# Performance work log

Measured on AMD Instinct MI355X. Metric: run time of the kernel, lower is better.

## Reference

```python
import jax, jax.numpy as jnp
import numpy as np

ALPHA = 0.2  # LeakyReLU negative slope
N, F_IN, F_OUT = 8192, 512, 64
NEG_INF = -9e15


def setup_inputs() -> dict:
    key = jax.random.key(0)
    k1, k2, k3, k4 = jax.random.split(key, 4)
    inp = jax.random.normal(k1, (N, F_IN), dtype=jnp.float32)
    adj = jax.random.randint(k2, (N, N), 0, 2, dtype=jnp.int32)
    W = jax.random.normal(k3, (F_IN, F_OUT), dtype=jnp.float32) * (1.414 / np.sqrt(F_IN))
    a = jax.random.normal(k4, (2 * F_OUT, 1), dtype=jnp.float32) * 0.1
    return {"input": inp, "adj": adj, "W": W, "a": a, "sparse": 0}


def reference(input, adj, W, a, sparse):
    h = input @ W  # [N, F_out]
    # Decompose concat([h_i, h_j]) @ a into additive src/dst terms (same math,
    # avoids the O(N^2 * 2F) intermediate): e_ij = leakyrelu(h_i@a1 + h_j@a2)
    f_src = h @ a[:F_OUT]   # [N, 1]
    f_dst = h @ a[F_OUT:]   # [N, 1]
    e = jax.nn.leaky_relu(f_src + f_dst.T, ALPHA)  # [N, N]
    attention = jnp.where(adj > 0, e, NEG_INF)
    attention = jax.nn.softmax(attention, axis=1)
    h_prime = attention @ h  # [N, F_out]
    return jax.nn.leaky_relu(h_prime, 0.01)[None]  # concat=True path; default F.leaky_relu slope 0.01
```

## Files before the change

kernel.cpp:

```cpp
#include <hip/hip_runtime.h>
#include <hip/hip_bf16.h>

#define N 8192
#define FIN 512
#define FOUT 64
#define ALPHA 0.2f

typedef __bf16 bf16x8 __attribute__((ext_vector_type(8)));
typedef float f32x4 __attribute__((ext_vector_type(4)));
typedef int i32x4 __attribute__((ext_vector_type(4)));

constexpr int JC = 512;
constexpr int NCH = N / JC;
constexpr int STR = JC + 8;


__device__ __forceinline__ unsigned enc_f(float x) {
    unsigned u = __float_as_uint(x);
    return (u & 0x80000000u) ? ~u : (u | 0x80000000u);
}
__device__ __forceinline__ float dec_f(unsigned u) {
    return (u & 0x80000000u) ? __uint_as_float(u & 0x7FFFFFFFu) : __uint_as_float(~u);
}

__global__ __launch_bounds__(64) void k_wt(const float* __restrict__ W,
                                           __bf16* __restrict__ WtG) {
    const int g = blockIdx.x * 64 + threadIdx.x;
    const int k = g >> 3;
    const int f0 = (g & 7) * 8;
    const float4 w0 = *(const float4*)(W + (size_t)k * FOUT + f0);
    const float4 w1 = *(const float4*)(W + (size_t)k * FOUT + f0 + 4);
    WtG[(size_t)(f0 + 0) * FIN + k] = (__bf16)w0.x;
    WtG[(size_t)(f0 + 1) * FIN + k] = (__bf16)w0.y;
    WtG[(size_t)(f0 + 2) * FIN + k] = (__bf16)w0.z;
    WtG[(size_t)(f0 + 3) * FIN + k] = (__bf16)w0.w;
    WtG[(size_t)(f0 + 4) * FIN + k] = (__bf16)w1.x;
    WtG[(size_t)(f0 + 5) * FIN + k] = (__bf16)w1.y;
    WtG[(size_t)(f0 + 6) * FIN + k] = (__bf16)w1.z;
    WtG[(size_t)(f0 + 7) * FIN + k] = (__bf16)w1.w;
}

__global__ __launch_bounds__(64) void k12(const float* __restrict__ in,
                                          const __bf16* __restrict__ WtG,
                                          const float* __restrict__ a,
                                          float* __restrict__ f_src,
                                          float* __restrict__ f_dst,
                                          unsigned* __restrict__ Mkey,
                                          __bf16* __restrict__ hT) {
    __shared__ __bf16 tb[64][16];
    const int lane = threadIdx.x;
    const int m = lane & 15, quad = lane >> 4;
    const int i0 = blockIdx.x * 16;

    f32x4 acc[4];
#pragma unroll
    for (int t = 0; t < 4; ++t) acc[t] = (f32x4){0.f, 0.f, 0.f, 0.f};

    const float* arow = in + (size_t)(i0 + m) * FIN + quad * 8;
    for (int k0 = 0; k0 < FIN; k0 += 32) {
        const float4 x0 = *(const float4*)(arow + k0);
        const float4 x1 = *(const float4*)(arow + k0 + 4);
        bf16x8 af;
        af[0] = (__bf16)x0.x; af[1] = (__bf16)x0.y; af[2] = (__bf16)x0.z; af[3] = (__bf16)x0.w;
        af[4] = (__bf16)x1.x; af[5] = (__bf16)x1.y; af[6] = (__bf16)x1.z; af[7] = (__bf16)x1.w;
#pragma unroll
        for (int t = 0; t < 4; ++t) {
            const bf16x8 bf = *(const bf16x8*)(WtG + (size_t)(t * 16 + m) * FIN + k0 + quad * 8);
            acc[t] = __builtin_amdgcn_mfma_f32_16x16x32_bf16(af, bf, acc[t], 0, 0, 0);
        }
    }
    float s1[4], s2[4];
#pragma unroll
    for (int r = 0; r < 4; ++r) { s1[r] = 0.f; s2[r] = 0.f; }
#pragma unroll
    for (int t = 0; t < 4; ++t) {
        const float a1 = a[t * 16 + m], a2 = a[64 + t * 16 + m];
#pragma unroll
        for (int r = 0; r < 4; ++r) {
            s1[r] += acc[t][r] * a1;
            s2[r] += acc[t][r] * a2;
        }
    }
#pragma unroll
    for (int off = 1; off <= 8; off <<= 1)
#pragma unroll
        for (int r = 0; r < 4; ++r) {
            s1[r] += __shfl_xor(s1[r], off);
            s2[r] += __shfl_xor(s2[r], off);
        }
    float lm = -1e30f;
    if (m == 0) {
#pragma unroll
        for (int r = 0; r < 4; ++r) {
            f_src[i0 + quad * 4 + r] = s1[r];
            f_dst[i0 + quad * 4 + r] = s2[r];
            lm = fmaxf(lm, s2[r]);
        }
    }
    lm = fmaxf(lm, __shfl_xor(lm, 16));
    lm = fmaxf(lm, __shfl_xor(lm, 32));
    if (lane == 0) atomicMax(Mkey, enc_f(lm));

#pragma unroll
    for (int t = 0; t < 4; ++t)
#pragma unroll
        for (int r = 0; r < 4; ++r) tb[t * 16 + m][quad * 4 + r] = (__bf16)acc[t][r];
    __syncthreads();
    {
        const int f = lane;
        const bf16x8 v0 = *(const bf16x8*)&tb[f][0];
        const bf16x8 v1 = *(const bf16x8*)&tb[f][8];
        *(bf16x8*)(hT + (size_t)f * N + i0) = v0;
        *(bf16x8*)(hT + (size_t)f * N + i0 + 8) = v1;
    }
}

__global__ __launch_bounds__(256) void k3_attn(const int* __restrict__ adj,
                                               const float* __restrict__ f_src,
                                               const float* __restrict__ fdstG,
                                               const unsigned* __restrict__ Mkey,
                                               const __bf16* __restrict__ hT,
                                               float* __restrict__ pnum,
                                               float* __restrict__ plsum) {
    __shared__ __bf16 sh[64 * STR];
    __shared__ float sfd[JC];
    const int tid = threadIdx.x;
    const int wv = tid >> 6, lane = tid & 63;
    const int m = lane & 15, quad = lane >> 4;
    const int i0 = (blockIdx.x * 4 + wv) * 16;
    const int jc = blockIdx.y * JC;
    const float LOG2E = 1.44269504088896f;

#pragma unroll
    for (int c = tid; c < 64 * JC / 8; c += 256) {
        const int f = c >> 6, off = (c & 63) * 8;
        *(bf16x8*)&sh[f * STR + off] = *(const bf16x8*)(hT + (size_t)f * N + jc + off);
    }
    if (tid < JC / 4) *(f32x4*)&sfd[tid * 4] = *(const f32x4*)(fdstG + jc + tid * 4);
    __syncthreads();

    const float M = dec_f(*Mkey);
    const float fs = f_src[i0 + m];
    const float t0 = fs + M;
    const float shift = fmaxf(t0, ALPHA * t0);

    f32x4 acc[4];
#pragma unroll
    for (int t = 0; t < 4; ++t) acc[t] = (f32x4){0.f, 0.f, 0.f, 0.f};
    f32x4 accl = (f32x4){0.f, 0.f, 0.f, 0.f};

    bf16x8 bones;
#pragma unroll
    for (int jj = 0; jj < 8; ++jj) bones[jj] = (__bf16)(m == 0 ? 1.0f : 0.0f);

    const int* arow = adj + (size_t)(i0 + m) * N + jc;

    i32x4 buf[3][4];
#pragma unroll
    for (int p = 0; p < 3; ++p) {
        const int* q = arow + p * 64 + quad * 8;
        buf[p][0] = __builtin_nontemporal_load((const i32x4*)q);
        buf[p][1] = __builtin_nontemporal_load((const i32x4*)(q + 4));
        buf[p][2] = __builtin_nontemporal_load((const i32x4*)(q + 32));
        buf[p][3] = __builtin_nontemporal_load((const i32x4*)(q + 36));
    }

#pragma unroll
    for (int it = 0; it < 8; ++it) {
        i32x4 cur[4];
#pragma unroll
        for (int x = 0; x < 4; ++x) cur[x] = buf[it % 3][x];
        if (it + 3 < 8) {
            const int* q = arow + (it + 3) * 64 + quad * 8;
            buf[it % 3][0] = __builtin_nontemporal_load((const i32x4*)q);
            buf[it % 3][1] = __builtin_nontemporal_load((const i32x4*)(q + 4));
            buf[it % 3][2] = __builtin_nontemporal_load((const i32x4*)(q + 32));
            buf[it % 3][3] = __builtin_nontemporal_load((const i32x4*)(q + 36));
        }
        const int jloc = it * 64;
#pragma unroll
        for (int u = 0; u < 2; ++u) {
            const i32x4 Aa = cur[u * 2], Ab = cur[u * 2 + 1];
            const f32x4 Da = *(const f32x4*)&sfd[jloc + u * 32 + quad * 8];
            const f32x4 Db = *(const f32x4*)&sfd[jloc + u * 32 + quad * 8 + 4];
            float wvv[8];
#pragma unroll
            for (int jj = 0; jj < 8; ++jj) {
                const float fd = jj < 4 ? Da[jj] : Db[jj - 4];
                const int am = jj < 4 ? Aa[jj] : Ab[jj - 4];
                float e = fs + fd;
                e = fmaxf(e, ALPHA * e);
                const float ex = __builtin_amdgcn_exp2f((e - shift) * LOG2E);
                wvv[jj] = am > 0 ? ex : 0.f;
            }
            bf16x8 af;
#pragma unroll
            for (int jj = 0; jj < 8; ++jj) af[jj] = (__bf16)wvv[jj];
#pragma unroll
            for (int t = 0; t < 4; ++t) {
                const bf16x8 bfr =
                    *(const bf16x8*)&sh[(t * 16 + m) * STR + jloc + u * 32 + quad * 8];
                acc[t] = __builtin_amdgcn_mfma_f32_16x16x32_bf16(af, bfr, acc[t], 0, 0, 0);
            }
            accl = __builtin_amdgcn_mfma_f32_16x16x32_bf16(af, bones, accl, 0, 0, 0);
        }
    }

    float* pn = pnum + (size_t)blockIdx.y * N * FOUT;
#pragma unroll
    for (int t = 0; t < 4; ++t)
#pragma unroll
        for (int r = 0; r < 4; ++r)
            pn[(size_t)(i0 + quad * 4 + r) * FOUT + t * 16 + m] = acc[t][r];
    if (m == 0) {
#pragma unroll
        for (int r = 0; r < 4; ++r)
            plsum[(size_t)blockIdx.y * N + i0 + quad * 4 + r] = accl[r];
    }
}

__global__ __launch_bounds__(256) void k4_norm(const float* __restrict__ pnum,
                                               const float* __restrict__ plsum,
                                               float* __restrict__ out) {
    const int idx = blockIdx.x * 256 + threadIdx.x;
    const int row = idx >> 6;
    float s = 0.f, l = 0.f;
#pragma unroll
    for (int c = 0; c < NCH; ++c) {
        s += pnum[(size_t)c * N * FOUT + idx];
        l += plsum[(size_t)c * N + row];
    }
    const float v = s / (l > 0.f ? l : 1.f);
    out[idx] = v > 0.f ? v : 0.01f * v;
}

extern "C" void kernel_launch(void* const* d_in, const int* in_sizes, int n_in,
                              void* d_out, int out_size, void* d_ws, size_t ws_size,
                              hipStream_t stream) {
    const float* in = (const float*)d_in[0];
    const int* adj = (const int*)d_in[1];
    const float* W = (const float*)d_in[2];
    const float* a = (const float*)d_in[3];
    float* out = (float*)d_out;

    char* ws = (char*)d_ws;
    unsigned* Mkey = (unsigned*)ws;
    float* f_src = (float*)(ws + 4096);
    float* f_dst = (float*)(ws + 36864);
    __bf16* WtG = (__bf16*)(ws + 69632);
    __bf16* hT = (__bf16*)(ws + 135168);
    float* plsum = (float*)(ws + 2097152);
    float* pnum = (float*)(ws + 4194304);

    hipMemsetAsync(ws, 0, 64, stream);

    k_wt<<<64, 64, 0, stream>>>(W, WtG);
    k12<<<N / 16, 64, 0, stream>>>(in, WtG, a, f_src, f_dst, Mkey, hT);

    dim3 g3(N / 64, NCH);
    k3_attn<<<g3, 256, 0, stream>>>(adj, f_src, f_dst, Mkey, hT, pnum, plsum);
    k4_norm<<<(N * FOUT) / 256, 256, 0, stream>>>(pnum, plsum, out);
}
```

Before: 428.0 us.

## Coalesce adjacency loads row-wise and stage attention weights through LDS

The attention kernel now reads adj one row at a time, with each lane loading 4 contiguous ints, so every wave fetches a full 1 KB row segment instead of strided 32-byte pieces spread across 16 rows. It computes the exp weights in that row-major layout, writes them to a per-wave LDS tile, then rereads them in MFMA A-fragment layout. Each block now loops over 4 column chunks of 256, so partial sums drop from 16 chunks to 8 and k4 has less reduction traffic. In exchange the change adds LDS round trips and extra __syncthreads per chunk, and it removes the register-prefetch pipelining of adj loads.

```diff
diff --git a/kernel.cpp b/kernel.cpp
--- a/kernel.cpp
+++ b/kernel.cpp
@@ -7,12 +7,14 @@
 #define ALPHA 0.2f
 
 typedef __bf16 bf16x8 __attribute__((ext_vector_type(8)));
+typedef __bf16 bf16x4 __attribute__((ext_vector_type(4)));
 typedef float f32x4 __attribute__((ext_vector_type(4)));
 typedef int i32x4 __attribute__((ext_vector_type(4)));
 
-constexpr int JC = 512;
-constexpr int NCH = N / JC;
-constexpr int STR = JC + 8;
+constexpr int JCH = 256;
+constexpr int CPB = 4;
+constexpr int NCH = 8;
+constexpr int HSTR = JCH + 8;
 
 
 __device__ __forceinline__ unsigned enc_f(float x) {
@@ -122,27 +124,25 @@
                                                const __bf16* __restrict__ hT,
                                                float* __restrict__ pnum,
                                                float* __restrict__ plsum) {
-    __shared__ __bf16 sh[64 * STR];
-    __shared__ float sfd[JC];
+    __shared__ __bf16 sh[64 * HSTR];
+    __shared__ __bf16 wlds[4 * 16 * HSTR];
     const int tid = threadIdx.x;
     const int wv = tid >> 6, lane = tid & 63;
     const int m = lane & 15, quad = lane >> 4;
-    const int i0 = (blockIdx.x * 4 + wv) * 16;
-    const int jc = blockIdx.y * JC;
+    const int i0w = (blockIdx.x * 4 + wv) * 16;
+    const int jb = blockIdx.y * (JCH * CPB);
     const float LOG2E = 1.44269504088896f;
-
-#pragma unroll
-    for (int c = tid; c < 64 * JC / 8; c += 256) {
-        const int f = c >> 6, off = (c & 63) * 8;
-        *(bf16x8*)&sh[f * STR + off] = *(const bf16x8*)(hT + (size_t)f * N + jc + off);
-    }
-    if (tid < JC / 4) *(f32x4*)&sfd[tid * 4] = *(const f32x4*)(fdstG + jc + tid * 4);
-    __syncthreads();
+    const int wbase = wv * 16 * HSTR;
 
     const float M = dec_f(*Mkey);
-    const float fs = f_src[i0 + m];
-    const float t0 = fs + M;
-    const float shift = fmaxf(t0, ALPHA * t0);
+    float fsr_a[16], shr_a[16];
+#pragma unroll
+    for (int r = 0; r < 16; ++r) {
+        const float fsr = f_src[i0w + r];
+        const float tt = fsr + M;
+        fsr_a[r] = fsr;
+        shr_a[r] = fmaxf(tt, ALPHA * tt);
+    }
 
     f32x4 acc[4];
 #pragma unroll
@@ -153,53 +153,41 @@
 #pragma unroll
     for (int jj = 0; jj < 8; ++jj) bones[jj] = (__bf16)(m == 0 ? 1.0f : 0.0f);
 
-    const int* arow = adj + (size_t)(i0 + m) * N + jc;
-
-    i32x4 buf[3][4];
-#pragma unroll
-    for (int p = 0; p < 3; ++p) {
-        const int* q = arow + p * 64 + quad * 8;
-        buf[p][0] = __builtin_nontemporal_load((const i32x4*)q);
-        buf[p][1] = __builtin_nontemporal_load((const i32x4*)(q + 4));
-        buf[p][2] = __builtin_nontemporal_load((const i32x4*)(q + 32));
-        buf[p][3] = __builtin_nontemporal_load((const i32x4*)(q + 36));
-    }
-
-#pragma unroll
-    for (int it = 0; it < 8; ++it) {
-        i32x4 cur[4];
-#pragma unroll
-        for (int x = 0; x < 4; ++x) cur[x] = buf[it % 3][x];
-        if (it + 3 < 8) {
-            const int* q = arow + (it + 3) * 64 + quad * 8;
-            buf[it % 3][0] = __builtin_nontemporal_load((const i32x4*)q);
-            buf[it % 3][1] = __builtin_nontemporal_load((const i32x4*)(q + 4));
-            buf[it % 3][2] = __builtin_nontemporal_load((const i32x4*)(q + 32));
-            buf[it % 3][3] = __builtin_nontemporal_load((const i32x4*)(q + 36));
-        }
-        const int jloc = it * 64;
-#pragma unroll
-        for (int u = 0; u < 2; ++u) {
-            const i32x4 Aa = cur[u * 2], Ab = cur[u * 2 + 1];
-            const f32x4 Da = *(const f32x4*)&sfd[jloc + u * 32 + quad * 8];
-            const f32x4 Db = *(const f32x4*)&sfd[jloc + u * 32 + quad * 8 + 4];
-            float wvv[8];
-#pragma unroll
-            for (int jj = 0; jj < 8; ++jj) {
-                const float fd = jj < 4 ? Da[jj] : Db[jj - 4];
-                const int am = jj < 4 ? Aa[jj] : Ab[jj - 4];
-                float e = fs + fd;
+    for (int c = 0; c < CPB; ++c) {
+        const int jc = jb + c * JCH;
+        __syncthreads();
+
+#pragma unroll
+        for (int k = 0; k < 8; ++k) {
+            const int s = tid + k * 256;
+            const int f = s >> 5, off = (s & 31) * 8;
+            *(bf16x8*)&sh[f * HSTR + off] = *(const bf16x8*)(hT + (size_t)f * N + jc + off);
+        }
+
+        const f32x4 fd = *(const f32x4*)(fdstG + jc + lane * 4);
+#pragma unroll
+        for (int r = 0; r < 16; ++r) {
+            const i32x4 am = __builtin_nontemporal_load(
+                (const i32x4*)(adj + (size_t)(i0w + r) * N + jc + lane * 4));
+            const float fsr = fsr_a[r], sh_r = shr_a[r];
+            bf16x4 w4;
+#pragma unroll
+            for (int jj = 0; jj < 4; ++jj) {
+                float e = fsr + fd[jj];
                 e = fmaxf(e, ALPHA * e);
-                const float ex = __builtin_amdgcn_exp2f((e - shift) * LOG2E);
-                wvv[jj] = am > 0 ? ex : 0.f;
+                const float ex = __builtin_amdgcn_exp2f((e - sh_r) * LOG2E);
+                w4[jj] = (__bf16)(am[jj] > 0 ? ex : 0.f);
             }
-            bf16x8 af;
-#pragma unroll
-            for (int jj = 0; jj < 8; ++jj) af[jj] = (__bf16)wvv[jj];
+            *(bf16x4*)&wlds[wbase + r * HSTR + lane * 4] = w4;
+        }
+        __syncthreads();
+
+#pragma unroll
+        for (int s = 0; s < 8; ++s) {
+            const bf16x8 af = *(const bf16x8*)&wlds[wbase + m * HSTR + s * 32 + quad * 8];
 #pragma unroll
             for (int t = 0; t < 4; ++t) {
-                const bf16x8 bfr =
-                    *(const bf16x8*)&sh[(t * 16 + m) * STR + jloc + u * 32 + quad * 8];
+                const bf16x8 bfr = *(const bf16x8*)&sh[(t * 16 + m) * HSTR + s * 32 + quad * 8];
                 acc[t] = __builtin_amdgcn_mfma_f32_16x16x32_bf16(af, bfr, acc[t], 0, 0, 0);
             }
             accl = __builtin_amdgcn_mfma_f32_16x16x32_bf16(af, bones, accl, 0, 0, 0);
@@ -211,11 +199,11 @@
     for (int t = 0; t < 4; ++t)
 #pragma unroll
         for (int r = 0; r < 4; ++r)
-            pn[(size_t)(i0 + quad * 4 + r) * FOUT + t * 16 + m] = acc[t][r];
+            pn[(size_t)(i0w + quad * 4 + r) * FOUT + t * 16 + m] = acc[t][r];
     if (m == 0) {
 #pragma unroll
         for (int r = 0; r < 4; ++r)
-            plsum[(size_t)blockIdx.y * N + i0 + quad * 4 + r] = accl[r];
+            plsum[(size_t)blockIdx.y * N + i0w + quad * 4 + r] = accl[r];
     }
 }
 
```

After: 465.7 us. +8.8%, slower.
